# Performance work log

Measured on AMD Instinct MI355X. Metric: run time of the kernel, lower is better.

## Reference

```python
import jax, jax.numpy as jnp
import numpy as np

NEG_INF = -1e9


def setup_inputs() -> dict:
    key = jax.random.key(0)
    ks = jax.random.split(key, 6)
    B, S, E, D = 32, 2048, 1024, 1024
    dec_hidden = jax.random.normal(ks[0], (B, D), dtype=jnp.float32)
    enc_outputs = jax.random.normal(ks[1], (B, S, E), dtype=jnp.float32)
    mask = jax.random.randint(ks[2], (B, S), 0, 2, dtype=jnp.int32)
    # scale weights ~ Glorot-ish so tanh isn't saturated
    W_enc = jax.random.normal(ks[3], (D, E), dtype=jnp.float32) / np.sqrt(E)
    W_dec = jax.random.normal(ks[4], (D, D), dtype=jnp.float32) / np.sqrt(D)
    v = jax.random.normal(ks[5], (D,), dtype=jnp.float32) / np.sqrt(D)
    return {"dec_hidden": dec_hidden, "enc_outputs": enc_outputs, "mask": mask,
            "W_enc": W_enc, "W_dec": W_dec, "v": v}


def reference(dec_hidden, enc_outputs, mask, W_enc, W_dec, v):
    # dh: [B, D]  (torch Linear: x @ W.T)
    dh = dec_hidden @ W_dec.T
    # eh: [B, S, D]
    eh = jnp.einsum('bse,de->bsd', enc_outputs, W_enc)
    # additive energy + projection by v -> scores [B, S]
    energy = jnp.tanh(dh[:, None, :] + eh)
    scores = jnp.einsum('bsd,d->bs', energy, v)
    scores = jnp.where(mask == 0, NEG_INF, scores)
    weights = jax.nn.softmax(scores, axis=1)          # [B, S]
    context = jnp.einsum('bs,bse->be', weights, enc_outputs)  # [B, E]
    return context, weights
```

## Files before the change

### kernel.cpp

```cpp
#include <hip/hip_runtime.h>
#include <stdint.h>

#define NEG_INF -1e9f

typedef float f32x4 __attribute__((ext_vector_type(4)));
typedef short bf16x8 __attribute__((ext_vector_type(8)));
typedef unsigned short ushort8 __attribute__((ext_vector_type(8)));

__device__ __forceinline__ unsigned short f2bf(float x) {
  union { float f; uint32_t u; } c; c.f = x;
  return (unsigned short)((c.u + 0x8000u) >> 16);
}

__global__ void prep_w_k(const float* __restrict__ W, unsigned short* __restrict__ Wt) {
  int t = blockIdx.x * 256 + threadIdx.x;
  int d  = t >> 7;
  int e0 = (t & 127) << 3;
  const float* src = W + ((size_t)d << 10) + e0;
  f32x4 f0 = *(const f32x4*)src;
  f32x4 f1 = *(const f32x4*)(src + 4);
  ushort8 u;
  u[0]=f2bf(f0[0]); u[1]=f2bf(f0[1]); u[2]=f2bf(f0[2]); u[3]=f2bf(f0[3]);
  u[4]=f2bf(f1[0]); u[5]=f2bf(f1[1]); u[6]=f2bf(f1[2]); u[7]=f2bf(f1[3]);
  int nt = d >> 7, r = d & 127, kt = e0 >> 5, c = e0 & 31;
  *(ushort8*)(Wt + (((size_t)(nt * 32 + kt)) << 12) + r * 32 + c) = u;
}

__global__ void prep_dh_k(const float* __restrict__ dec, const float* __restrict__ Wd,
                          float* __restrict__ dh) {
  __shared__ float sdec[1024];
  int b = blockIdx.x >> 2;
  for (int i = threadIdx.x; i < 1024; i += 256) sdec[i] = dec[(b << 10) + i];
  __syncthreads();
  int d = ((blockIdx.x & 3) << 8) + threadIdx.x;
  const float* wr = Wd + ((size_t)d << 10);
  float a = 0.f;
  for (int k = 0; k < 1024; k += 4) {
    f32x4 wv = *(const f32x4*)(wr + k);
    f32x4 xv = *(const f32x4*)(&sdec[k]);
    a += wv[0]*xv[0] + wv[1]*xv[1] + wv[2]*xv[2] + wv[3]*xv[3];
  }
  dh[(b << 10) + d] = a;
}

__global__ void compact_k(const int* __restrict__ mask, int* __restrict__ rows,
                          int* __restrict__ cnt, float* __restrict__ wout) {
  int b = blockIdx.x, tid = threadIdx.x;
  int lane = tid & 63, wv = tid >> 6;
  int mloc[8]; int c = 0;
  #pragma unroll
  for (int ii = 0; ii < 8; ++ii) {
    int s = tid * 8 + ii;
    int m = mask[(b << 11) + s];
    mloc[ii] = m; c += m;
    wout[(b << 11) + s] = 0.f;
  }
  int inc = c;
  #pragma unroll
  for (int off = 1; off < 64; off <<= 1) {
    int nn = __shfl_up(inc, off);
    if (lane >= off) inc += nn;
  }
  __shared__ int wsum[4];
  if (lane == 63) wsum[wv] = inc;
  __syncthreads();
  int base = 0;
  for (int w = 0; w < wv; ++w) base += wsum[w];
  int idx = base + inc - c;
  #pragma unroll
  for (int ii = 0; ii < 8; ++ii) {
    if (mloc[ii]) { rows[(b << 11) + idx] = tid * 8 + ii; ++idx; }
  }
  if (tid == 0) cnt[b] = wsum[0] + wsum[1] + wsum[2] + wsum[3];
}

__global__ void pack_k(const float* __restrict__ enc, const int* __restrict__ rows,
                       const int* __restrict__ cnt, unsigned short* __restrict__ encP) {
  int b = blockIdx.x >> 4, mt = blockIdx.x & 15;
  int n = cnt[b];
  if (mt * 128 >= n) return;
  __shared__ int sr[128];
  if (threadIdx.x < 128) {
    int i = mt * 128 + threadIdx.x; if (i >= n) i = n - 1;
    sr[threadIdx.x] = rows[(b << 11) + i];
  }
  __syncthreads();
  unsigned short* dst = encP + ((size_t)(b * 16 + mt) << 17);
  for (int it = 0; it < 64; ++it) {
    int chunk = it * 256 + threadIdx.x;
    int ir = chunk >> 7;
    int e0 = (chunk & 127) << 3;
    const float* src = enc + (((size_t)(b << 11) + sr[ir]) << 10) + e0;
    f32x4 f0 = *(const f32x4*)src;
    f32x4 f1 = *(const f32x4*)(src + 4);
    ushort8 u;
    u[0]=f2bf(f0[0]); u[1]=f2bf(f0[1]); u[2]=f2bf(f0[2]); u[3]=f2bf(f0[3]);
    u[4]=f2bf(f1[0]); u[5]=f2bf(f1[1]); u[6]=f2bf(f1[2]); u[7]=f2bf(f1[3]);
    int kt = e0 >> 5, cc = e0 & 31;
    *(ushort8*)(dst + kt * 4096 + ir * 32 + cc) = u;
  }
}

template<bool PACKED>
__global__ __launch_bounds__(256) void score2_k(
    const float* __restrict__ enc, const unsigned short* __restrict__ encP,
    const unsigned short* __restrict__ Wt, const float* __restrict__ dh,
    const float* __restrict__ v, const int* __restrict__ rows,
    const int* __restrict__ cnt, float* __restrict__ pscores)
{
  int xcd = blockIdx.x & 7;
  int pos = blockIdx.x >> 3;
  int L   = xcd * 512 + pos;
  int bt  = L >> 3, nt = L & 7;
  int b   = bt >> 4, mt = bt & 15;
  int n0  = nt << 7;
  int cb_cnt = cnt[b];
  if (mt * 128 >= cb_cnt) return;

  __shared__ __align__(16) unsigned short As[2][128][32];
  __shared__ __align__(16) unsigned short Bs[2][128][32];
  __shared__ float sc[128][2];
  __shared__ int srow[128];

  int tid  = threadIdx.x;
  int lane = tid & 63;
  int wave = tid >> 6;
  int wm = wave >> 1, wn = wave & 1;

  const float* agp0 = nullptr;
  const float* agp1 = nullptr;
  if constexpr (!PACKED) {
    if (tid < 128) {
      int i = mt * 128 + tid; if (i >= cb_cnt) i = cb_cnt - 1;
      srow[tid] = rows[(b << 11) + i];
    }
    __syncthreads();
    int r0 = tid >> 2, c = (tid & 3) << 3;
    agp0 = enc + (((size_t)(b << 11) + srow[r0])      << 10) + c;
    agp1 = enc + (((size_t)(b << 11) + srow[r0 + 64]) << 10) + c;
  }
  const unsigned short* atile = nullptr;
  if constexpr (PACKED) atile = encP + ((size_t)(b * 16 + mt) << 17);

  f32x4 acc[4][4];
  #pragma unroll
  for (int i = 0; i < 4; ++i)
    #pragma unroll
    for (int j = 0; j < 4; ++j)
      acc[i][j] = (f32x4){0.f, 0.f, 0.f, 0.f};

  auto stage = [&](int bi, int kt) {
    if constexpr (PACKED) {
      const unsigned short* ta = atile + ((size_t)kt << 12);
      #pragma unroll
      for (int j = 0; j < 2; ++j) {
        int chunk = wave * 2 + j;
        const unsigned short* g = ta + chunk * 512 + lane * 8;
        void* l = (void*)(&As[bi][0][0] + chunk * 512);
        __builtin_amdgcn_global_load_lds((__attribute__((address_space(1))) void*)(void*)g,
                                         (__attribute__((address_space(3))) void*)l, 16, 0, 0);
      }
    } else {
      int k0 = kt << 5;
      int r0 = tid >> 2, c = (tid & 3) << 3;
      {
        f32x4 f0 = *(const f32x4*)(agp0 + k0);
        f32x4 f1 = *(const f32x4*)(agp0 + k0 + 4);
        ushort8 u;
        u[0]=f2bf(f0[0]); u[1]=f2bf(f0[1]); u[2]=f2bf(f0[2]); u[3]=f2bf(f0[3]);
        u[4]=f2bf(f1[0]); u[5]=f2bf(f1[1]); u[6]=f2bf(f1[2]); u[7]=f2bf(f1[3]);
        *(ushort8*)&As[bi][r0][c] = u;
      }
      {
        f32x4 f0 = *(const f32x4*)(agp1 + k0);
        f32x4 f1 = *(const f32x4*)(agp1 + k0 + 4);
        ushort8 u;
        u[0]=f2bf(f0[0]); u[1]=f2bf(f0[1]); u[2]=f2bf(f0[2]); u[3]=f2bf(f0[3]);
        u[4]=f2bf(f1[0]); u[5]=f2bf(f1[1]); u[6]=f2bf(f1[2]); u[7]=f2bf(f1[3]);
        *(ushort8*)&As[bi][r0 + 64][c] = u;
      }
    }
    const unsigned short* tb = Wt + (((size_t)(nt * 32 + kt)) << 12);
    #pragma unroll
    for (int j = 0; j < 2; ++j) {
      int chunk = wave * 2 + j;
      const unsigned short* g = tb + chunk * 512 + lane * 8;
      void* l = (void*)(&Bs[bi][0][0] + chunk * 512);
      __builtin_amdgcn_global_load_lds((__attribute__((address_space(1))) void*)(void*)g,
                                       (__attribute__((address_space(3))) void*)l, 16, 0, 0);
    }
  };

  auto compute = [&](int bi) {
    bf16x8 a[4], bb[4];
    #pragma unroll
    for (int i = 0; i < 4; ++i)
      a[i] = *(const bf16x8*)&As[bi][wm * 64 + i * 16 + (lane & 15)][(lane >> 4) << 3];
    #pragma unroll
    for (int j = 0; j < 4; ++j)
      bb[j] = *(const bf16x8*)&Bs[bi][wn * 64 + j * 16 + (lane & 15)][(lane >> 4) << 3];
    #pragma unroll
    for (int i = 0; i < 4; ++i)
      #pragma unroll
      for (int j = 0; j < 4; ++j)
        acc[i][j] = __builtin_amdgcn_mfma_f32_16x16x32_bf16(a[i], bb[j], acc[i][j], 0, 0, 0);
  };

  stage(0, 0);
  __syncthreads();
  int bi = 0;
  for (int kt = 0; kt < 31; ++kt) {
    stage(bi ^ 1, kt + 1);
    compute(bi);
    __syncthreads();
    bi ^= 1;
  }
  compute(bi);

  int cb = n0 + wn * 64 + (lane & 15);
  float vv[4], dd[4];
  #pragma unroll
  for (int j = 0; j < 4; ++j) {
    int dcol = cb + j * 16;
    vv[j] = v[dcol];
    dd[j] = dh[(b << 10) + dcol];
  }
  #pragma unroll
  for (int i = 0; i < 4; ++i) {
    #pragma unroll
    for (int r = 0; r < 4; ++r) {
      float p = 0.f;
      #pragma unroll
      for (int j = 0; j < 4; ++j) {
        float x = acc[i][j][r] + dd[j];
        float e = __expf(2.0f * x);
        float t = 1.0f - __fdividef(2.0f, e + 1.0f);
        p += vv[j] * t;
      }
      p += __shfl_xor(p, 1); p += __shfl_xor(p, 2);
      p += __shfl_xor(p, 4); p += __shfl_xor(p, 8);
      if ((lane & 15) == 0)
        sc[wm * 64 + i * 16 + ((lane >> 4) << 2) + r][wn] = p;
    }
  }
  __syncthreads();
  if (tid < 128) {
    int i = mt * 128 + tid;
    if (i < cb_cnt)
      pscores[((size_t)nt << 16) + (b << 11) + i] = sc[tid][0] + sc[tid][1];
  }
}

__global__ void softmax2_k(const float* __restrict__ ps, const int* __restrict__ rows,
                           const int* __restrict__ cnt, float* __restrict__ wout,
                           float* __restrict__ wc) {
  int b = blockIdx.x;
  int tid = threadIdx.x;
  int n = cnt[b];
  float val[8];
  float m = -INFINITY;
  #pragma unroll
  for (int ii = 0; ii < 8; ++ii) {
    int i = tid + ii * 256;
    float s = -INFINITY;
    if (i < n) {
      s = 0.f;
      #pragma unroll
      for (int nt = 0; nt < 8; ++nt) s += ps[((size_t)nt << 16) + (b << 11) + i];
    }
    val[ii] = s;
    m = fmaxf(m, s);
  }
  #pragma unroll
  for (int off = 1; off < 64; off <<= 1) m = fmaxf(m, __shfl_xor(m, off));
  __shared__ float r1[4], r2[4];
  if ((tid & 63) == 0) r1[tid >> 6] = m;
  __syncthreads();
  m = fmaxf(fmaxf(r1[0], r1[1]), fmaxf(r1[2], r1[3]));
  float ssum = 0.f;
  #pragma unroll
  for (int ii = 0; ii < 8; ++ii) { val[ii] = __expf(val[ii] - m); ssum += val[ii]; }
  #pragma unroll
  for (int off = 1; off < 64; off <<= 1) ssum += __shfl_xor(ssum, off);
  if ((tid & 63) == 0) r2[tid >> 6] = ssum;
  __syncthreads();
  ssum = r2[0] + r2[1] + r2[2] + r2[3];
  float inv = 1.0f / ssum;
  #pragma unroll
  for (int ii = 0; ii < 8; ++ii) {
    int i = tid + ii * 256;
    if (i < n) {
      float w = val[ii] * inv;
      wc[(b << 11) + i] = w;
      wout[((size_t)b << 11) + rows[(b << 11) + i]] = w;
    }
  }
}

__global__ void ctx2_k(const float* __restrict__ enc, const float* __restrict__ wc,
                       const int* __restrict__ rows, const int* __restrict__ cnt,
                       float* __restrict__ cp) {
  int bb = blockIdx.x;
  int b = bb >> 4, ch = bb & 15;
  int n = cnt[b];
  int i0 = ch << 7;
  __shared__ float sw[128];
  __shared__ int sr[128];
  if (threadIdx.x < 128) {
    int i = i0 + threadIdx.x;
    sw[threadIdx.x] = (i < n) ? wc[(b << 11) + i] : 0.f;
    int ic = (i < n) ? i : (n - 1);
    sr[threadIdx.x] = rows[(b << 11) + ic];
  }
  __syncthreads();
  int nv = n - i0; if (nv > 128) nv = 128; if (nv < 0) nv = 0;
  int e0 = threadIdx.x << 2;
  f32x4 acc = {0.f, 0.f, 0.f, 0.f};
  for (int s = 0; s < nv; ++s) {
    const float* base = enc + ((((size_t)(b << 11)) + sr[s]) << 10) + e0;
    f32x4 x = *(const f32x4*)base;
    float w = sw[s];
    acc[0] += w * x[0]; acc[1] += w * x[1]; acc[2] += w * x[2]; acc[3] += w * x[3];
  }
  *(f32x4*)(cp + ((size_t)bb << 10) + e0) = acc;
}

__global__ void ctx_red_k(const float* __restrict__ cp, float* __restrict__ out) {
  int t = blockIdx.x * 256 + threadIdx.x;
  int b = t >> 10, e = t & 1023;
  float a = 0.f;
  #pragma unroll
  for (int ch = 0; ch < 16; ++ch) a += cp[(((size_t)(b * 16 + ch)) << 10) + e];
  out[t] = a;
}

extern "C" void kernel_launch(void* const* d_in, const int* in_sizes, int n_in,
                              void* d_out, int out_size, void* d_ws, size_t ws_size,
                              hipStream_t stream) {
  const float* dec  = (const float*)d_in[0];
  const float* enc  = (const float*)d_in[1];
  const int*   mask = (const int*)d_in[2];
  const float* Wenc = (const float*)d_in[3];
  const float* Wdec = (const float*)d_in[4];
  const float* v    = (const float*)d_in[5];
  float* out_ctx = (float*)d_out;
  float* out_w   = (float*)d_out + 32768;

  char* ws = (char*)d_ws;
  unsigned short* Wt = (unsigned short*)ws;
  float* dh    = (float*)(ws + (2u << 20));
  int*   rows  = (int*)(ws + (2u << 20) + (128u << 10));
  float* wc    = (float*)(ws + (2u << 20) + (384u << 10));
  int*   cnt   = (int*)(ws + (2u << 20) + (640u << 10));
  float* pscores = (float*)(ws + (3u << 20));
  float* cp      = (float*)(ws + (3u << 20));
  unsigned short* encP = (unsigned short*)(ws + (8ull << 20));

  bool fast = ws_size >= (136ull << 20);

  hipLaunchKernelGGL(prep_w_k,   dim3(512), dim3(256), 0, stream, Wenc, Wt);
  hipLaunchKernelGGL(prep_dh_k,  dim3(128), dim3(256), 0, stream, dec, Wdec, dh);
  hipLaunchKernelGGL(compact_k,  dim3(32),  dim3(256), 0, stream, mask, rows, cnt, out_w);
  if (fast) {
    hipLaunchKernelGGL(pack_k,          dim3(512),  dim3(256), 0, stream, enc, rows, cnt, encP);
    hipLaunchKernelGGL(score2_k<true>,  dim3(4096), dim3(256), 0, stream, enc, encP, Wt, dh, v, rows, cnt, pscores);
  } else {
    hipLaunchKernelGGL(score2_k<false>, dim3(4096), dim3(256), 0, stream, enc, encP, Wt, dh, v, rows, cnt, pscores);
  }
  hipLaunchKernelGGL(softmax2_k, dim3(32),  dim3(256), 0, stream, pscores, rows, cnt, out_w, wc);
  hipLaunchKernelGGL(ctx2_k,     dim3(512), dim3(256), 0, stream, enc, wc, rows, cnt, cp);
  hipLaunchKernelGGL(ctx_red_k,  dim3(128), dim3(256), 0, stream, cp, out_ctx);
}
```

Baseline: 228.3 us.

## Enlarge score GEMM tiles with 4-stage swizzled pipeline and bf16 context pass

The score GEMM moves to 256x256 tiles with 512 threads and a 4-deep global_load_lds pipeline. Loads are interleaved between MFMA halves with explicit vmcnt waits, s_setprio and barriers. Both operands use an XOR-swizzled bf16 layout to avoid LDS bank conflicts. The context reduction now reads the packed bf16 encoder tiles instead of re-gathering fp32 rows, which halves that traffic but computes the context from bf16-rounded inputs. The unpacked fallback path for small workspaces is removed.

```diff
diff --git a/kernel.cpp b/kernel.cpp
--- a/kernel.cpp
+++ b/kernel.cpp
@@ -1,7 +1,5 @@
 #include <hip/hip_runtime.h>
 #include <stdint.h>
-
-#define NEG_INF -1e9f
 
 typedef float f32x4 __attribute__((ext_vector_type(4)));
 typedef short bf16x8 __attribute__((ext_vector_type(8)));
@@ -11,19 +9,25 @@
   union { float f; uint32_t u; } c; c.f = x;
   return (unsigned short)((c.u + 0x8000u) >> 16);
 }
-
-__global__ void prep_w_k(const float* __restrict__ W, unsigned short* __restrict__ Wt) {
+__device__ __forceinline__ float bf2f(unsigned short u) {
+  union { uint32_t u; float f; } c; c.u = ((uint32_t)u) << 16;
+  return c.f;
+}
+
+__global__ void prep_w3_k(const float* __restrict__ W, unsigned short* __restrict__ Wt) {
   int t = blockIdx.x * 256 + threadIdx.x;
   int d  = t >> 7;
-  int e0 = (t & 127) << 3;
-  const float* src = W + ((size_t)d << 10) + e0;
+  int c0 = (t & 127) << 3;
+  const float* src = W + ((size_t)d << 10) + c0;
   f32x4 f0 = *(const f32x4*)src;
   f32x4 f1 = *(const f32x4*)(src + 4);
   ushort8 u;
   u[0]=f2bf(f0[0]); u[1]=f2bf(f0[1]); u[2]=f2bf(f0[2]); u[3]=f2bf(f0[3]);
   u[4]=f2bf(f1[0]); u[5]=f2bf(f1[1]); u[6]=f2bf(f1[2]); u[7]=f2bf(f1[3]);
-  int nt = d >> 7, r = d & 127, kt = e0 >> 5, c = e0 & 31;
-  *(ushort8*)(Wt + (((size_t)(nt * 32 + kt)) << 12) + r * 32 + c) = u;
+  int nt = d >> 8, rr = d & 255;
+  int kt = c0 >> 5;
+  int q  = ((c0 & 31) >> 3) ^ ((rr >> 1) & 3);
+  *(ushort8*)(Wt + (((size_t)nt) << 18) + kt * 8192 + rr * 32 + q * 8) = u;
 }
 
 __global__ void prep_dh_k(const float* __restrict__ dec, const float* __restrict__ Wd,
@@ -74,184 +78,197 @@
   if (tid == 0) cnt[b] = wsum[0] + wsum[1] + wsum[2] + wsum[3];
 }
 
-__global__ void pack_k(const float* __restrict__ enc, const int* __restrict__ rows,
-                       const int* __restrict__ cnt, unsigned short* __restrict__ encP) {
-  int b = blockIdx.x >> 4, mt = blockIdx.x & 15;
+__global__ void pack3_k(const float* __restrict__ enc, const int* __restrict__ rows,
+                        const int* __restrict__ cnt, unsigned short* __restrict__ encP) {
+  int b = blockIdx.x >> 3, mt = blockIdx.x & 7;
   int n = cnt[b];
-  if (mt * 128 >= n) return;
-  __shared__ int sr[128];
-  if (threadIdx.x < 128) {
-    int i = mt * 128 + threadIdx.x; if (i >= n) i = n - 1;
+  if (mt * 256 >= n) return;
+  __shared__ int sr[256];
+  if (threadIdx.x < 256) {
+    int i = mt * 256 + threadIdx.x; if (i >= n) i = n - 1;
     sr[threadIdx.x] = rows[(b << 11) + i];
   }
   __syncthreads();
-  unsigned short* dst = encP + ((size_t)(b * 16 + mt) << 17);
-  for (int it = 0; it < 64; ++it) {
-    int chunk = it * 256 + threadIdx.x;
-    int ir = chunk >> 7;
-    int e0 = (chunk & 127) << 3;
-    const float* src = enc + (((size_t)(b << 11) + sr[ir]) << 10) + e0;
+  unsigned short* dst = encP + (((size_t)(b * 8 + mt)) << 18);
+  for (int it = 0; it < 128; ++it) {
+    int idx = it * 256 + threadIdx.x;
+    int r   = idx >> 7;
+    int c0  = (idx & 127) << 3;
+    const float* src = enc + (((size_t)(b << 11) + sr[r]) << 10) + c0;
     f32x4 f0 = *(const f32x4*)src;
     f32x4 f1 = *(const f32x4*)(src + 4);
     ushort8 u;
     u[0]=f2bf(f0[0]); u[1]=f2bf(f0[1]); u[2]=f2bf(f0[2]); u[3]=f2bf(f0[3]);
     u[4]=f2bf(f1[0]); u[5]=f2bf(f1[1]); u[6]=f2bf(f1[2]); u[7]=f2bf(f1[3]);
-    int kt = e0 >> 5, cc = e0 & 31;
-    *(ushort8*)(dst + kt * 4096 + ir * 32 + cc) = u;
-  }
-}
-
-template<bool PACKED>
-__global__ __launch_bounds__(256) void score2_k(
-    const float* __restrict__ enc, const unsigned short* __restrict__ encP,
-    const unsigned short* __restrict__ Wt, const float* __restrict__ dh,
-    const float* __restrict__ v, const int* __restrict__ rows,
+    int kt = c0 >> 5;
+    int q  = ((c0 & 31) >> 3) ^ ((r >> 1) & 3);
+    *(ushort8*)(dst + kt * 8192 + r * 32 + q * 8) = u;
+  }
+}
+
+#define BAR() __builtin_amdgcn_s_barrier()
+#define SBAR() __builtin_amdgcn_sched_barrier(0)
+
+struct KtCtx {
+  const unsigned short* aT;
+  const unsigned short* bT;
+  unsigned short* AS;
+  unsigned short* BS;
+  int so;
+  int ldso;
+};
+
+__device__ __forceinline__ void stage_chunk(const unsigned short* gbase, unsigned short* lbase) {
+  __builtin_amdgcn_global_load_lds((const __attribute__((address_space(1))) void*)(const void*)gbase,
+                                   (__attribute__((address_space(3))) void*)(void*)lbase, 16, 0, 0);
+}
+__device__ __forceinline__ void stageA(const KtCtx& c, int kt, int half) {
+  stage_chunk(c.aT + (((size_t)kt) << 13) + (half << 12) + c.so,
+              c.AS + ((kt & 3) << 13) + (half << 12) + c.ldso);
+}
+__device__ __forceinline__ void stageB(const KtCtx& c, int kt, int half) {
+  stage_chunk(c.bT + (((size_t)kt) << 13) + (half << 12) + c.so,
+              c.BS + ((kt & 3) << 13) + (half << 12) + c.ldso);
+}
+
+template<int FN, bool S0, bool S1>
+__device__ __forceinline__ void ktile_body(const KtCtx& c, int kt,
+                                           const int* offA, const int* offB,
+                                           f32x4 (&acc)[8][4]) {
+  const unsigned short* as = c.AS + ((kt & 3) << 13);
+  const unsigned short* bs = c.BS + ((kt & 3) << 13);
+  bf16x8 a0[4], bb[4];
+  #pragma unroll
+  for (int i = 0; i < 4; ++i) a0[i] = *(const bf16x8*)(as + offA[i]);
+  #pragma unroll
+  for (int j = 0; j < 4; ++j) bb[j] = *(const bf16x8*)(bs + offB[j]);
+  if constexpr (S0) { stageB(c, kt + 2, 0); stageB(c, kt + 2, 1); }
+  BAR();
+  __builtin_amdgcn_s_setprio(1);
+  #pragma unroll
+  for (int i = 0; i < 4; ++i)
+    #pragma unroll
+    for (int j = 0; j < 4; ++j)
+      acc[i][j] = __builtin_amdgcn_mfma_f32_16x16x32_bf16(a0[i], bb[j], acc[i][j], 0, 0, 0);
+  __builtin_amdgcn_s_setprio(0);
+  BAR();
+  bf16x8 a1[4];
+  #pragma unroll
+  for (int i = 0; i < 4; ++i) a1[i] = *(const bf16x8*)(as + offA[4 + i]);
+  if constexpr (S1) { stageA(c, kt + 3, 0); stageA(c, kt + 3, 1); }
+  BAR();
+  __builtin_amdgcn_s_setprio(1);
+  #pragma unroll
+  for (int i = 0; i < 4; ++i)
+    #pragma unroll
+    for (int j = 0; j < 4; ++j)
+      acc[4 + i][j] = __builtin_amdgcn_mfma_f32_16x16x32_bf16(a1[i], bb[j], acc[4 + i][j], 0, 0, 0);
+  __builtin_amdgcn_s_setprio(0);
+  SBAR();
+  if constexpr (FN == 6)      asm volatile("s_waitcnt vmcnt(6)" ::: "memory");
+  else if constexpr (FN == 4) asm volatile("s_waitcnt vmcnt(4)" ::: "memory");
+  else if constexpr (FN == 0) asm volatile("s_waitcnt vmcnt(0)" ::: "memory");
+  BAR();
+  SBAR();
+}
+
+__global__ __launch_bounds__(512, 2) void score3_k(
+    const unsigned short* __restrict__ encP, const unsigned short* __restrict__ Wt,
+    const float* __restrict__ dh, const float* __restrict__ v,
     const int* __restrict__ cnt, float* __restrict__ pscores)
 {
-  int xcd = blockIdx.x & 7;
-  int pos = blockIdx.x >> 3;
-  int L   = xcd * 512 + pos;
-  int bt  = L >> 3, nt = L & 7;
-  int b   = bt >> 4, mt = bt & 15;
-  int n0  = nt << 7;
-  int cb_cnt = cnt[b];
-  if (mt * 128 >= cb_cnt) return;
-
-  __shared__ __align__(16) unsigned short As[2][128][32];
-  __shared__ __align__(16) unsigned short Bs[2][128][32];
-  __shared__ float sc[128][2];
-  __shared__ int srow[128];
+  int L  = (blockIdx.x & 7) * 128 + (blockIdx.x >> 3);
+  int b  = L >> 5, mt = (L >> 2) & 7, nt = L & 3;
+  int n  = cnt[b];
+  if (mt * 256 >= n) return;
+
+  __shared__ __align__(16) unsigned short SMEM[65536];
+  unsigned short* AS = SMEM;
+  unsigned short* BS = SMEM + 32768;
 
   int tid  = threadIdx.x;
   int lane = tid & 63;
-  int wave = tid >> 6;
-  int wm = wave >> 1, wn = wave & 1;
-
-  const float* agp0 = nullptr;
-  const float* agp1 = nullptr;
-  if constexpr (!PACKED) {
-    if (tid < 128) {
-      int i = mt * 128 + tid; if (i >= cb_cnt) i = cb_cnt - 1;
-      srow[tid] = rows[(b << 11) + i];
-    }
-    __syncthreads();
-    int r0 = tid >> 2, c = (tid & 3) << 3;
-    agp0 = enc + (((size_t)(b << 11) + srow[r0])      << 10) + c;
-    agp1 = enc + (((size_t)(b << 11) + srow[r0 + 64]) << 10) + c;
-  }
-  const unsigned short* atile = nullptr;
-  if constexpr (PACKED) atile = encP + ((size_t)(b * 16 + mt) << 17);
-
-  f32x4 acc[4][4];
-  #pragma unroll
-  for (int i = 0; i < 4; ++i)
+  int wv   = tid >> 6;
+  int wm   = wv >> 2, wn = wv & 3;
+  int l15  = lane & 15, l4 = lane >> 4;
+
+  KtCtx c;
+  c.aT = encP + (((size_t)(b * 8 + mt)) << 18);
+  c.bT = Wt + (((size_t)nt) << 18);
+  c.AS = AS; c.BS = BS;
+  c.so = tid * 8;
+  c.ldso = wv * 512;
+
+  int offA[8], offB[4];
+  #pragma unroll
+  for (int mf = 0; mf < 8; ++mf) {
+    int rr = wm * 128 + mf * 16 + l15;
+    offA[mf] = rr * 32 + ((l4 ^ (rr >> 1)) & 3) * 8;
+  }
+  #pragma unroll
+  for (int nf = 0; nf < 4; ++nf) {
+    int rn = wn * 64 + nf * 16 + l15;
+    offB[nf] = rn * 32 + ((l4 ^ (rn >> 1)) & 3) * 8;
+  }
+
+  f32x4 acc[8][4];
+  #pragma unroll
+  for (int i = 0; i < 8; ++i)
     #pragma unroll
     for (int j = 0; j < 4; ++j)
       acc[i][j] = (f32x4){0.f, 0.f, 0.f, 0.f};
 
-  auto stage = [&](int bi, int kt) {
-    if constexpr (PACKED) {
-      const unsigned short* ta = atile + ((size_t)kt << 12);
-      #pragma unroll
-      for (int j = 0; j < 2; ++j) {
-        int chunk = wave * 2 + j;
-        const unsigned short* g = ta + chunk * 512 + lane * 8;
-        void* l = (void*)(&As[bi][0][0] + chunk * 512);
-        __builtin_amdgcn_global_load_lds((__attribute__((address_space(1))) void*)(void*)g,
-                                         (__attribute__((address_space(3))) void*)l, 16, 0, 0);
-      }
-    } else {
-      int k0 = kt << 5;
-      int r0 = tid >> 2, c = (tid & 3) << 3;
-      {
-        f32x4 f0 = *(const f32x4*)(agp0 + k0);
-        f32x4 f1 = *(const f32x4*)(agp0 + k0 + 4);
-        ushort8 u;
-        u[0]=f2bf(f0[0]); u[1]=f2bf(f0[1]); u[2]=f2bf(f0[2]); u[3]=f2bf(f0[3]);
-        u[4]=f2bf(f1[0]); u[5]=f2bf(f1[1]); u[6]=f2bf(f1[2]); u[7]=f2bf(f1[3]);
-        *(ushort8*)&As[bi][r0][c] = u;
-      }
-      {
-        f32x4 f0 = *(const f32x4*)(agp1 + k0);
-        f32x4 f1 = *(const f32x4*)(agp1 + k0 + 4);
-        ushort8 u;
-        u[0]=f2bf(f0[0]); u[1]=f2bf(f0[1]); u[2]=f2bf(f0[2]); u[3]=f2bf(f0[3]);
-        u[4]=f2bf(f1[0]); u[5]=f2bf(f1[1]); u[6]=f2bf(f1[2]); u[7]=f2bf(f1[3]);
-        *(ushort8*)&As[bi][r0 + 64][c] = u;
-      }
-    }
-    const unsigned short* tb = Wt + (((size_t)(nt * 32 + kt)) << 12);
-    #pragma unroll
-    for (int j = 0; j < 2; ++j) {
-      int chunk = wave * 2 + j;
-      const unsigned short* g = tb + chunk * 512 + lane * 8;
-      void* l = (void*)(&Bs[bi][0][0] + chunk * 512);
-      __builtin_amdgcn_global_load_lds((__attribute__((address_space(1))) void*)(void*)g,
-                                       (__attribute__((address_space(3))) void*)l, 16, 0, 0);
-    }
-  };
-
-  auto compute = [&](int bi) {
-    bf16x8 a[4], bb[4];
-    #pragma unroll
-    for (int i = 0; i < 4; ++i)
-      a[i] = *(const bf16x8*)&As[bi][wm * 64 + i * 16 + (lane & 15)][(lane >> 4) << 3];
-    #pragma unroll
-    for (int j = 0; j < 4; ++j)
-      bb[j] = *(const bf16x8*)&Bs[bi][wn * 64 + j * 16 + (lane & 15)][(lane >> 4) << 3];
-    #pragma unroll
-    for (int i = 0; i < 4; ++i)
-      #pragma unroll
-      for (int j = 0; j < 4; ++j)
-        acc[i][j] = __builtin_amdgcn_mfma_f32_16x16x32_bf16(a[i], bb[j], acc[i][j], 0, 0, 0);
-  };
-
-  stage(0, 0);
-  __syncthreads();
-  int bi = 0;
-  for (int kt = 0; kt < 31; ++kt) {
-    stage(bi ^ 1, kt + 1);
-    compute(bi);
-    __syncthreads();
-    bi ^= 1;
-  }
-  compute(bi);
-
-  int cb = n0 + wn * 64 + (lane & 15);
+  stageA(c, 0, 0); stageA(c, 0, 1); stageB(c, 0, 0); stageB(c, 0, 1);
+  stageA(c, 1, 0); stageA(c, 1, 1); stageB(c, 1, 0); stageB(c, 1, 1);
+  stageA(c, 2, 0); stageA(c, 2, 1);
+  SBAR();
+  asm volatile("s_waitcnt vmcnt(6)" ::: "memory");
+  BAR();
+  SBAR();
+
+  int kt = 0;
+  for (; kt < 29; ++kt) ktile_body<6, true, true>(c, kt, offA, offB, acc);
+  ktile_body<4, true,  false>(c, 29, offA, offB, acc);
+  ktile_body<0, false, false>(c, 30, offA, offB, acc);
+  ktile_body<-1, false, false>(c, 31, offA, offB, acc);
+
+  float* sc = (float*)BS;
   float vv[4], dd[4];
   #pragma unroll
-  for (int j = 0; j < 4; ++j) {
-    int dcol = cb + j * 16;
-    vv[j] = v[dcol];
-    dd[j] = dh[(b << 10) + dcol];
-  }
-  #pragma unroll
-  for (int i = 0; i < 4; ++i) {
+  for (int nf = 0; nf < 4; ++nf) {
+    int dcol = nt * 256 + wn * 64 + nf * 16 + l15;
+    vv[nf] = v[dcol];
+    dd[nf] = dh[(b << 10) + dcol];
+  }
+  #pragma unroll
+  for (int mf = 0; mf < 8; ++mf) {
     #pragma unroll
     for (int r = 0; r < 4; ++r) {
       float p = 0.f;
       #pragma unroll
-      for (int j = 0; j < 4; ++j) {
-        float x = acc[i][j][r] + dd[j];
+      for (int nf = 0; nf < 4; ++nf) {
+        float x = acc[mf][nf][r] + dd[nf];
         float e = __expf(2.0f * x);
         float t = 1.0f - __fdividef(2.0f, e + 1.0f);
-        p += vv[j] * t;
+        p += vv[nf] * t;
       }
       p += __shfl_xor(p, 1); p += __shfl_xor(p, 2);
       p += __shfl_xor(p, 4); p += __shfl_xor(p, 8);
-      if ((lane & 15) == 0)
-        sc[wm * 64 + i * 16 + ((lane >> 4) << 2) + r][wn] = p;
+      if (l15 == 0)
+        sc[(wm * 128 + mf * 16 + (l4 << 2) + r) * 4 + wn] = p;
     }
   }
   __syncthreads();
-  if (tid < 128) {
-    int i = mt * 128 + tid;
-    if (i < cb_cnt)
-      pscores[((size_t)nt << 16) + (b << 11) + i] = sc[tid][0] + sc[tid][1];
-  }
-}
-
-__global__ void softmax2_k(const float* __restrict__ ps, const int* __restrict__ rows,
+  if (tid < 256) {
+    int i = mt * 256 + tid;
+    if (i < n) {
+      float s = sc[tid * 4 + 0] + sc[tid * 4 + 1] + sc[tid * 4 + 2] + sc[tid * 4 + 3];
+      pscores[(((size_t)nt) << 16) + (b << 11) + i] = s;
+    }
+  }
+}
+
+__global__ void softmax3_k(const float* __restrict__ ps, const int* __restrict__ rows,
                            const int* __restrict__ cnt, float* __restrict__ wout,
                            float* __restrict__ wc) {
   int b = blockIdx.x;
@@ -266,7 +283,7 @@
     if (i < n) {
       s = 0.f;
       #pragma unroll
-      for (int nt = 0; nt < 8; ++nt) s += ps[((size_t)nt << 16) + (b << 11) + i];
+      for (int nt = 0; nt < 4; ++nt) s += ps[(((size_t)nt) << 16) + (b << 11) + i];
     }
     val[ii] = s;
     m = fmaxf(m, s);
@@ -297,40 +314,56 @@
   }
 }
 
-__global__ void ctx2_k(const float* __restrict__ enc, const float* __restrict__ wc,
-                       const int* __restrict__ rows, const int* __restrict__ cnt,
-                       float* __restrict__ cp) {
-  int bb = blockIdx.x;
-  int b = bb >> 4, ch = bb & 15;
+__global__ void ctx3_k(const unsigned short* __restrict__ encP, const float* __restrict__ wc,
+                       const int* __restrict__ cnt, float* __restrict__ cp) {
+  int b = blockIdx.x >> 3, mt = blockIdx.x & 7;
   int n = cnt[b];
-  int i0 = ch << 7;
-  __shared__ float sw[128];
-  __shared__ int sr[128];
-  if (threadIdx.x < 128) {
-    int i = i0 + threadIdx.x;
-    sw[threadIdx.x] = (i < n) ? wc[(b << 11) + i] : 0.f;
-    int ic = (i < n) ? i : (n - 1);
-    sr[threadIdx.x] = rows[(b << 11) + ic];
-  }
-  __syncthreads();
-  int nv = n - i0; if (nv > 128) nv = 128; if (nv < 0) nv = 0;
-  int e0 = threadIdx.x << 2;
-  f32x4 acc = {0.f, 0.f, 0.f, 0.f};
-  for (int s = 0; s < nv; ++s) {
-    const float* base = enc + ((((size_t)(b << 11)) + sr[s]) << 10) + e0;
-    f32x4 x = *(const f32x4*)base;
-    float w = sw[s];
-    acc[0] += w * x[0]; acc[1] += w * x[1]; acc[2] += w * x[2]; acc[3] += w * x[3];
-  }
-  *(f32x4*)(cp + ((size_t)bb << 10) + e0) = acc;
-}
-
-__global__ void ctx_red_k(const float* __restrict__ cp, float* __restrict__ out) {
+  float* out = cp + (((size_t)(b * 8 + mt)) << 10);
+  int tid = threadIdx.x;
+  if (mt * 256 >= n) {
+    #pragma unroll
+    for (int j = 0; j < 4; ++j) out[tid * 4 + j] = 0.f;
+    return;
+  }
+  __shared__ float sw[256];
+  __shared__ float red[128][8];
+  if (tid < 256) {
+    int i = mt * 256 + tid;
+    sw[tid] = (i < n) ? wc[(b << 11) + i] : 0.f;
+  }
+  __syncthreads();
+  const unsigned short* tile = encP + (((size_t)(b * 8 + mt)) << 18);
+  int cb8  = tid & 127;
+  int half = tid >> 7;
+  int kt = cb8 >> 2, qlog = cb8 & 3;
+  float a[8];
+  #pragma unroll
+  for (int j = 0; j < 8; ++j) a[j] = 0.f;
+  int r0 = half * 128;
+  for (int rr = 0; rr < 128; ++rr) {
+    int r = r0 + rr;
+    float w = sw[r];
+    ushort8 u = *(const ushort8*)(tile + kt * 8192 + r * 32 + ((qlog ^ (r >> 1)) & 3) * 8);
+    #pragma unroll
+    for (int j = 0; j < 8; ++j) a[j] += w * bf2f(u[j]);
+  }
+  if (half == 1) {
+    #pragma unroll
+    for (int j = 0; j < 8; ++j) red[cb8][j] = a[j];
+  }
+  __syncthreads();
+  if (half == 0) {
+    #pragma unroll
+    for (int j = 0; j < 8; ++j) out[cb8 * 8 + j] = a[j] + red[cb8][j];
+  }
+}
+
+__global__ void ctx_red3_k(const float* __restrict__ cp, float* __restrict__ out) {
   int t = blockIdx.x * 256 + threadIdx.x;
   int b = t >> 10, e = t & 1023;
   float a = 0.f;
   #pragma unroll
-  for (int ch = 0; ch < 16; ++ch) a += cp[(((size_t)(b * 16 + ch)) << 10) + e];
+  for (int mt = 0; mt < 8; ++mt) a += cp[(((size_t)(b * 8 + mt)) << 10) + e];
   out[t] = a;
 }
 
@@ -353,21 +386,15 @@
   float* wc    = (float*)(ws + (2u << 20) + (384u << 10));
   int*   cnt   = (int*)(ws + (2u << 20) + (640u << 10));
   float* pscores = (float*)(ws + (3u << 20));
-  float* cp      = (float*)(ws + (3u << 20));
+  float* cp      = (float*)(ws + (5u << 20));
   unsigned short* encP = (unsigned short*)(ws + (8ull << 20));
 
-  bool fast = ws_size >= (136ull << 20);
-
-  hipLaunchKernelGGL(prep_w_k,   dim3(512), dim3(256), 0, stream, Wenc, Wt);
-  hipLaunchKernelGGL(prep_dh_k,  dim3(128), dim3(256), 0, stream, dec, Wdec, dh);
-  hipLaunchKernelGGL(compact_k,  dim3(32),  dim3(256), 0, stream, mask, rows, cnt, out_w);
-  if (fast) {
-    hipLaunchKernelGGL(pack_k,          dim3(512),  dim3(256), 0, stream, enc, rows, cnt, encP);
-    hipLaunchKernelGGL(score2_k<true>,  dim3(4096), dim3(256), 0, stream, enc, encP, Wt, dh, v, rows, cnt, pscores);
-  } else {
-    hipLaunchKernelGGL(score2_k<false>, dim3(4096), dim3(256), 0, stream, enc, encP, Wt, dh, v, rows, cnt, pscores);
-  }
-  hipLaunchKernelGGL(softmax2_k, dim3(32),  dim3(256), 0, stream, pscores, rows, cnt, out_w, wc);
-  hipLaunchKernelGGL(ctx2_k,     dim3(512), dim3(256), 0, stream, enc, wc, rows, cnt, cp);
-  hipLaunchKernelGGL(ctx_red_k,  dim3(128), dim3(256), 0, stream, cp, out_ctx);
-}
+  hipLaunchKernelGGL(prep_w3_k,  dim3(512),  dim3(256), 0, stream, Wenc, Wt);
+  hipLaunchKernelGGL(prep_dh_k,  dim3(128),  dim3(256), 0, stream, dec, Wdec, dh);
+  hipLaunchKernelGGL(compact_k,  dim3(32),   dim3(256), 0, stream, mask, rows, cnt, out_w);
+  hipLaunchKernelGGL(pack3_k,    dim3(256),  dim3(256), 0, stream, enc, rows, cnt, encP);
+  hipLaunchKernelGGL(score3_k,   dim3(1024), dim3(512), 0, stream, encP, Wt, dh, v, cnt, pscores);
+  hipLaunchKernelGGL(softmax3_k, dim3(32),   dim3(256), 0, stream, pscores, rows, cnt, out_w, wc);
+  hipLaunchKernelGGL(ctx3_k,     dim3(256),  dim3(256), 0, stream, encP, wc, cnt, cp);
+  hipLaunchKernelGGL(ctx_red3_k, dim3(128),  dim3(256), 0, stream, cp, out_ctx);
+}
```

Result: slower. 246.6 us (+8.0%).
